# Kernel optimization log

Measured on AMD Instinct MI355X. Metric: run time of the kernel, lower is better.

The kernel has to match this reference:

```python
import jax, jax.numpy as jnp
import numpy as np
import math

QUERY_DIM = 1024
KEY_DIM = 768
VALUE_DIM = 768
NUM_HEADS = 16
HEAD_DIM = QUERY_DIM // NUM_HEADS


def setup_inputs() -> dict:
    key = jax.random.key(0)
    ks = jax.random.split(key, 11)
    B, Sq, Skv = 4, 2048, 2048
    query = jax.random.normal(ks[0], (B, Sq, QUERY_DIM), dtype=jnp.float32)
    k_in = jax.random.normal(ks[1], (B, Skv, KEY_DIM), dtype=jnp.float32)
    v_in = jax.random.normal(ks[2], (B, Skv, VALUE_DIM), dtype=jnp.float32)
    # Linear weights stored as [in, out] (y = x @ W + b), equivalent to torch's x @ W^T.
    def lin(k, fan_in, fan_out):
        bound = 1.0 / math.sqrt(fan_in)
        kw, kb = jax.random.split(k)
        W = jax.random.uniform(kw, (fan_in, fan_out), minval=-bound, maxval=bound, dtype=jnp.float32)
        b = jax.random.uniform(kb, (fan_out,), minval=-bound, maxval=bound, dtype=jnp.float32)
        return W, b
    Wq, bq = lin(ks[3], QUERY_DIM, QUERY_DIM)
    Wk, bk = lin(ks[4], KEY_DIM, QUERY_DIM)
    Wv, bv = lin(ks[5], VALUE_DIM, QUERY_DIM)
    Wo, bo = lin(ks[6], QUERY_DIM, QUERY_DIM)
    return {"query": query, "key": k_in, "value": v_in,
            "Wq": Wq, "bq": bq, "Wk": Wk, "bk": bk,
            "Wv": Wv, "bv": bv, "Wo": Wo, "bo": bo}


def reference(query, key, value, Wq, bq, Wk, bk, Wv, bv, Wo, bo):
    B, Sq, _ = query.shape
    H, D = NUM_HEADS, HEAD_DIM
    # Projections -> [B, H, S, D]
    Q = (query @ Wq + bq).reshape(B, Sq, H, D).transpose(0, 2, 1, 3)
    K = (key @ Wk + bk).reshape(B, -1, H, D).transpose(0, 2, 1, 3)
    V = (value @ Wv + bv).reshape(B, -1, H, D).transpose(0, 2, 1, 3)
    scale = 1.0 / math.sqrt(D)
    scores = jnp.einsum('bhqd,bhkd->bhqk', Q, K) * scale  # [B,H,Sq,Skv]
    weights = jax.nn.softmax(scores, axis=-1)
    attended = jnp.einsum('bhqk,bhkd->bhqd', weights, V)
    attended = attended.transpose(0, 2, 1, 3).reshape(B, Sq, H * D)
    # torch .squeeze(1): no-op since Sq > 1
    return attended @ Wo + bo
```

## Files before the change

### kernel.cpp

```cpp
#include <hip/hip_runtime.h>

#define B_ 4
#define SQ 2048
#define SKV 2048
#define DMODEL 1024
#define DKV 768
#define NH 16
#define DH 64

typedef unsigned short u16;
typedef __bf16 bf16x4 __attribute__((ext_vector_type(4)));
typedef __bf16 bf16x8 __attribute__((ext_vector_type(8)));
typedef float f32x4 __attribute__((ext_vector_type(4)));
typedef float f32x16 __attribute__((ext_vector_type(16)));

__device__ __forceinline__ u16 f2bf(float f) {
  union { __bf16 b; u16 u; } cv;
  cv.b = (__bf16)f;
  return cv.u;
}

__device__ __forceinline__ unsigned cvtpk(float lo, float hi) {
  unsigned r;
  asm("v_cvt_pk_bf16_f32 %0, %1, %2" : "=v"(r) : "v"(lo), "v"(hi));
  return r;
}

__device__ __forceinline__ float fexp2(float x) {
  float r;
  asm("v_exp_f32 %0, %1" : "=v"(r) : "v"(x));
  return r;
}

#define GLDS(gp, lp) __builtin_amdgcn_global_load_lds(                         \
    (const __attribute__((address_space(1))) unsigned*)(gp),                   \
    (__attribute__((address_space(3))) unsigned*)(lp), 16, 0, 0)


__global__ __launch_bounds__(128)
void cast3_kernel(const float* __restrict__ Aq, const float* __restrict__ Ak,
                  const float* __restrict__ Av,
                  u16* __restrict__ Qb, u16* __restrict__ Kb, u16* __restrict__ Vb) {
  const int z = blockIdx.y;
  const float* src = (z == 0) ? Aq : (z == 1) ? Ak : Av;
  u16* dst = (z == 0) ? Qb : (z == 1) ? Kb : Vb;
  const int K = (z == 0) ? DMODEL : DKV;
  const int row = blockIdx.x;
  const int c8 = threadIdx.x * 8;
  if (c8 >= K) return;
  const float* s = src + (size_t)row * K + c8;
  float4 v0 = *(const float4*)s;
  float4 v1 = *(const float4*)(s + 4);
  union { bf16x4 b[2]; uint4 u; } cv;
  cv.b[0][0] = (__bf16)v0.x; cv.b[0][1] = (__bf16)v0.y;
  cv.b[0][2] = (__bf16)v0.z; cv.b[0][3] = (__bf16)v0.w;
  cv.b[1][0] = (__bf16)v1.x; cv.b[1][1] = (__bf16)v1.y;
  cv.b[1][2] = (__bf16)v1.z; cv.b[1][3] = (__bf16)v1.w;
  int kx = c8 ^ ((row & 7) << 3);
  *(uint4*)(dst + (size_t)row * K + kx) = cv.u;
}

__global__ __launch_bounds__(256)
void wt4_kernel(const float* __restrict__ W0, const float* __restrict__ W1,
                const float* __restrict__ W2, const float* __restrict__ W3,
                u16* __restrict__ T0, u16* __restrict__ T1,
                u16* __restrict__ T2, u16* __restrict__ T3) {
  const int z = blockIdx.z;
  const float* W = (z == 0) ? W0 : (z == 1) ? W1 : (z == 2) ? W2 : W3;
  u16* T = (z == 0) ? T0 : (z == 1) ? T1 : (z == 2) ? T2 : T3;
  const int K = (z == 1 || z == 2) ? DKV : DMODEL;
  const int N = DMODEL;
  int n0 = blockIdx.x * 32, k0 = blockIdx.y * 32;
  if (k0 >= K) return;
  __shared__ float tl[32][33];
  int tx = threadIdx.x, ty = threadIdx.y;
#pragma unroll
  for (int p = 0; p < 4; ++p)
    tl[ty + 8 * p][tx] = W[(size_t)(k0 + ty + 8 * p) * N + n0 + tx];
  __syncthreads();
#pragma unroll
  for (int p = 0; p < 4; ++p) {
    int n = n0 + ty + 8 * p;
    int kx = (k0 + tx) ^ ((n & 7) << 3);
    T[(size_t)n * K + kx] = f2bf(tl[tx][ty + 8 * p]);
  }
}

__global__ __launch_bounds__(256)
void qkv_kernel(const u16* __restrict__ Qbf, const u16* __restrict__ Kbf,
                const u16* __restrict__ Vbf,
                const u16* __restrict__ Wtq, const u16* __restrict__ Wtk,
                const u16* __restrict__ Wtv,
                const float* __restrict__ bq, const float* __restrict__ bk,
                const float* __restrict__ bv,
                float sclq,
                u16* __restrict__ Qp, u16* __restrict__ Kp, u16* __restrict__ Vt) {
  __shared__ __align__(16) u16 Alds[128][64];
  __shared__ __align__(16) u16 Blds[128][64];
  const int z = blockIdx.z;
  const u16* Ab = (z == 0) ? Qbf : (z == 1) ? Kbf : Vbf;
  const u16* Wt = (z == 0) ? Wtq : (z == 1) ? Wtk : Wtv;
  const float* bias = (z == 0) ? bq : (z == 1) ? bk : bv;
  const int K = (z == 0) ? DMODEL : DKV;
  const float oscale = (z == 0) ? sclq : 1.0f;

  const int t = threadIdx.x;
  const int l = t & 63;
  const int lx = l & 15, lg = l >> 4;
  const int wid = t >> 6;
  const int wr = wid >> 1, wc = wid & 1;

  int flat = blockIdx.y * 8 + blockIdx.x;
  int by = (flat & 7) * 8 + ((flat >> 3) & 7);
  int bx = flat >> 6;
  const int m0 = by * 128, n0 = bx * 128;

  const int srow = l >> 3;
  const int scol = (l & 7) * 8;
  const int swz = (lx & 7) << 3;

  f32x4 acc[4][4];
#pragma unroll
  for (int i = 0; i < 4; ++i)
#pragma unroll
    for (int j = 0; j < 4; ++j) acc[i][j] = (f32x4){0.f, 0.f, 0.f, 0.f};

  for (int k0 = 0; k0 < K; k0 += 64) {
    __syncthreads();
#pragma unroll
    for (int j = 0; j < 4; ++j) {
      int row = wid * 32 + j * 8;
      GLDS(Wt + (size_t)(n0 + row + srow) * K + k0 + scol, &Blds[row][0]);
      GLDS(Ab + (size_t)(m0 + row + srow) * K + k0 + scol, &Alds[row][0]);
    }
    __syncthreads();
#pragma unroll
    for (int kk = 0; kk < 64; kk += 32) {
      bf16x8 af[4], bfr[4];
#pragma unroll
      for (int i = 0; i < 4; ++i)
        af[i] = *(const bf16x8*)(&Alds[wr * 64 + i * 16 + lx][(kk + lg * 8) ^ swz]);
#pragma unroll
      for (int j = 0; j < 4; ++j)
        bfr[j] = *(const bf16x8*)(&Blds[wc * 64 + j * 16 + lx][(kk + lg * 8) ^ swz]);
#pragma unroll
      for (int i = 0; i < 4; ++i)
#pragma unroll
        for (int j = 0; j < 4; ++j)
          acc[i][j] = __builtin_amdgcn_mfma_f32_16x16x32_bf16(af[i], bfr[j], acc[i][j], 0, 0, 0);
    }
  }
#pragma unroll
  for (int j = 0; j < 4; ++j) {
    int col = n0 + wc * 64 + j * 16 + lx;
    float bv = bias[col];
#pragma unroll
    for (int i = 0; i < 4; ++i) {
      int rowb = m0 + wr * 64 + i * 16 + lg * 4;
      f32x4 c = acc[i][j];
      if (z == 2) {
        int b = rowb >> 11, s = rowb & 2047;
        int h = col >> 6, d = col & 63;
        u16* vt = Vt + (size_t)((b * NH + h) * DH + d) * SKV + s;
        union { bf16x4 v; uint2 u; } cv;
        cv.v[0] = (__bf16)(c[0] + bv); cv.v[1] = (__bf16)(c[1] + bv);
        cv.v[2] = (__bf16)(c[2] + bv); cv.v[3] = (__bf16)(c[3] + bv);
        *(uint2*)vt = cv.u;
      } else {
        u16* op = (z == 0) ? Qp : Kp;
#pragma unroll
        for (int r = 0; r < 4; ++r)
          op[(size_t)(rowb + r) * DMODEL + col] = f2bf((c[r] + bv) * oscale);
      }
    }
  }
}

__global__ __launch_bounds__(256)
void oproj_kernel(const u16* __restrict__ Ab, const u16* __restrict__ Wt,
                  const float* __restrict__ bias, float* __restrict__ out_) {
  const int N = DMODEL, K = DMODEL;
  __shared__ __align__(16) u16 Alds[128][64];
  __shared__ __align__(16) u16 Blds[128][64];
  const int t = threadIdx.x;
  const int l = t & 63;
  const int lx = l & 15, lg = l >> 4;
  const int wid = t >> 6;
  const int wr = wid >> 1, wc = wid & 1;

  int flat = blockIdx.y * 8 + blockIdx.x;
  int by = (flat & 7) * 8 + ((flat >> 3) & 7);
  int bx = flat >> 6;
  const int m0 = by * 128, n0 = bx * 128;

  const int srow = l >> 3;
  const int scol = (l & 7) * 8;
  const int swz = (lx & 7) << 3;

  f32x4 acc[4][4];
#pragma unroll
  for (int i = 0; i < 4; ++i)
#pragma unroll
    for (int j = 0; j < 4; ++j) acc[i][j] = (f32x4){0.f, 0.f, 0.f, 0.f};

  for (int k0 = 0; k0 < K; k0 += 64) {
    __syncthreads();
#pragma unroll
    for (int j = 0; j < 4; ++j) {
      int row = wid * 32 + j * 8;
      GLDS(Wt + (size_t)(n0 + row + srow) * K + k0 + scol, &Blds[row][0]);
      GLDS(Ab + (size_t)(m0 + row + srow) * K + k0 + scol, &Alds[row][0]);
    }
    __syncthreads();
#pragma unroll
    for (int kk = 0; kk < 64; kk += 32) {
      bf16x8 af[4], bfr[4];
#pragma unroll
      for (int i = 0; i < 4; ++i)
        af[i] = *(const bf16x8*)(&Alds[wr * 64 + i * 16 + lx][(kk + lg * 8) ^ swz]);
#pragma unroll
      for (int j = 0; j < 4; ++j)
        bfr[j] = *(const bf16x8*)(&Blds[wc * 64 + j * 16 + lx][(kk + lg * 8) ^ swz]);
#pragma unroll
      for (int i = 0; i < 4; ++i)
#pragma unroll
        for (int j = 0; j < 4; ++j)
          acc[i][j] = __builtin_amdgcn_mfma_f32_16x16x32_bf16(af[i], bfr[j], acc[i][j], 0, 0, 0);
    }
  }
#pragma unroll
  for (int j = 0; j < 4; ++j) {
    int col = n0 + wc * 64 + j * 16 + lx;
    float bv = bias[col];
#pragma unroll
    for (int i = 0; i < 4; ++i) {
      int rowb = m0 + wr * 64 + i * 16 + lg * 4;
      f32x4 c = acc[i][j];
#pragma unroll
      for (int r = 0; r < 4; ++r)
        out_[(size_t)(rowb + r) * N + col] = c[r] + bv;
    }
  }
}

#define KVB 64
#define KP 72

__global__ __launch_bounds__(512, 2)
void attn_kernel(const u16* __restrict__ Qp, const u16* __restrict__ Kp,
                 const u16* __restrict__ Vt, u16* __restrict__ Att) {
  __shared__ __align__(16) u16 Klds[2][KVB][KP];
  __shared__ __align__(16) u16 Vlds[2][DH][KP];
  const int t = threadIdx.x;
  const int l = t & 63;
  const int ql = l & 31, hi = l >> 5;
  const int wid = t >> 6;

  const int flat = blockIdx.y * 8 + blockIdx.x;
  const int xcd = flat & 7;
  const int rest = flat >> 3;
  const int bh = xcd * 8 + (rest & 7);
  const int qb = rest >> 3;
  const int b = bh >> 4, h = bh & 15;
  const int q = qb * 256 + wid * 32 + ql;

  bf16x8 qf[4];
  const u16* qbase = Qp + (size_t)(b * SQ + q) * DMODEL + h * 64 + hi * 8;
#pragma unroll
  for (int ds = 0; ds < 4; ++ds) qf[ds] = *(const bf16x8*)(qbase + ds * 16);

  bf16x8 ones;
  {
    union { unsigned u[4]; bf16x8 v; } o;
    o.u[0] = o.u[1] = o.u[2] = o.u[3] = 0x3F803F80u;
    ones = o.v;
  }
  f32x16 z16;
#pragma unroll
  for (int r = 0; r < 16; ++r) z16[r] = 0.f;

  f32x16 acc0, acc1, sacc;
#pragma unroll
  for (int r = 0; r < 16; ++r) { acc0[r] = 0.f; acc1[r] = 0.f; sacc[r] = 0.f; }

  const int sr = t >> 3;
  const int sc = (t & 7) * 8;
  const u16* kg = Kp + (size_t)(b * SKV) * DMODEL + h * 64;
  const u16* vg = Vt + ((size_t)(b * NH + h) * DH + sr) * SKV;

  {
    uint4 k0 = *(const uint4*)(kg + (size_t)sr * DMODEL + sc);
    uint4 v0 = *(const uint4*)(vg + sc);
    *(uint4*)(&Klds[0][sr][sc]) = k0;
    *(uint4*)(&Vlds[0][sr][sc]) = v0;
  }
  int cur = 0;

  for (int kv0 = 0; kv0 < SKV; kv0 += KVB) {
    uint4 kr0, vr0;
    const bool pf = (kv0 + KVB) < SKV;
    if (pf) {
      kr0 = *(const uint4*)(kg + (size_t)(kv0 + KVB + sr) * DMODEL + sc);
      vr0 = *(const uint4*)(vg + kv0 + KVB + sc);
    }
    __syncthreads();

    f32x16 st0, st1;
    __builtin_amdgcn_s_setprio(1);
    {
      bf16x8 k0 = *(const bf16x8*)(&Klds[cur][ql][hi * 8]);
      bf16x8 k1 = *(const bf16x8*)(&Klds[cur][32 + ql][hi * 8]);
      st0 = __builtin_amdgcn_mfma_f32_32x32x16_bf16(k0, qf[0], z16, 0, 0, 0);
      st1 = __builtin_amdgcn_mfma_f32_32x32x16_bf16(k1, qf[0], z16, 0, 0, 0);
    }
#pragma unroll
    for (int ds = 1; ds < 4; ++ds) {
      bf16x8 k0 = *(const bf16x8*)(&Klds[cur][ql][ds * 16 + hi * 8]);
      bf16x8 k1 = *(const bf16x8*)(&Klds[cur][32 + ql][ds * 16 + hi * 8]);
      st0 = __builtin_amdgcn_mfma_f32_32x32x16_bf16(k0, qf[ds], st0, 0, 0, 0);
      st1 = __builtin_amdgcn_mfma_f32_32x32x16_bf16(k1, qf[ds], st1, 0, 0, 0);
    }
    __builtin_amdgcn_s_setprio(0);

#pragma unroll
    for (int r = 0; r < 16; ++r) { st0[r] = fexp2(st0[r]); st1[r] = fexp2(st1[r]); }

    __builtin_amdgcn_s_setprio(1);
#pragma unroll
    for (int tt = 0; tt < 2; ++tt) {
      const f32x16& stt = tt ? st1 : st0;
      unsigned pk[8];
#pragma unroll
      for (int j = 0; j < 8; ++j) pk[j] = cvtpk(stt[2 * j], stt[2 * j + 1]);
#pragma unroll
      for (int ksl = 0; ksl < 2; ++ksl) {
        auto wA = __builtin_amdgcn_permlane32_swap(pk[4 * ksl + 0], pk[4 * ksl + 2], false, false);
        auto wB = __builtin_amdgcn_permlane32_swap(pk[4 * ksl + 1], pk[4 * ksl + 3], false, false);
        union { unsigned w[4]; bf16x8 v; } pfr;
        pfr.w[0] = (unsigned)wA[0]; pfr.w[1] = (unsigned)wB[0];
        pfr.w[2] = (unsigned)wA[1]; pfr.w[3] = (unsigned)wB[1];
        int ks = tt * 2 + ksl;
        bf16x8 v0 = *(const bf16x8*)(&Vlds[cur][ql][ks * 16 + hi * 8]);
        bf16x8 v1 = *(const bf16x8*)(&Vlds[cur][32 + ql][ks * 16 + hi * 8]);
        acc0 = __builtin_amdgcn_mfma_f32_32x32x16_bf16(v0, pfr.v, acc0, 0, 0, 0);
        acc1 = __builtin_amdgcn_mfma_f32_32x32x16_bf16(v1, pfr.v, acc1, 0, 0, 0);
        sacc = __builtin_amdgcn_mfma_f32_32x32x16_bf16(ones, pfr.v, sacc, 0, 0, 0);
      }
    }
    __builtin_amdgcn_s_setprio(0);

    if (pf) {
      int nxt = cur ^ 1;
      *(uint4*)(&Klds[nxt][sr][sc]) = kr0;
      *(uint4*)(&Vlds[nxt][sr][sc]) = vr0;
    }
    cur ^= 1;
  }

  float inv = 1.0f / sacc[0];
  u16* ob = Att + (size_t)(b * SQ + q) * DMODEL + h * 64;
  const int oswz = (ql & 7) << 3;
#pragma unroll
  for (int dt = 0; dt < 2; ++dt) {
    const f32x16& a = dt ? acc1 : acc0;
#pragma unroll
    for (int g = 0; g < 4; ++g) {
      unsigned w0 = cvtpk(a[4 * g] * inv, a[4 * g + 1] * inv);
      unsigned w1 = cvtpk(a[4 * g + 2] * inv, a[4 * g + 3] * inv);
      *(uint2*)(ob + ((dt * 32 + g * 8 + hi * 4) ^ oswz)) = make_uint2(w0, w1);
    }
  }
}

extern "C" void kernel_launch(void* const* d_in, const int* in_sizes, int n_in,
                              void* d_out, int out_size, void* d_ws, size_t ws_size,
                              hipStream_t stream) {
  const float* query = (const float*)d_in[0];
  const float* key   = (const float*)d_in[1];
  const float* value = (const float*)d_in[2];
  const float* Wq = (const float*)d_in[3];
  const float* bq = (const float*)d_in[4];
  const float* Wk = (const float*)d_in[5];
  const float* bk = (const float*)d_in[6];
  const float* Wv = (const float*)d_in[7];
  const float* bv = (const float*)d_in[8];
  const float* Wo = (const float*)d_in[9];
  const float* bo = (const float*)d_in[10];
  float* out = (float*)d_out;

  u16* ws = (u16*)d_ws;
  const size_t MTOK = (size_t)B_ * SQ;
  u16* Qp  = ws;
  u16* Kp  = Qp + MTOK * DMODEL;
  u16* Vtb = Kp + MTOK * DMODEL;
  u16* Att = Vtb + MTOK * DMODEL;
  u16* WqT = Att + MTOK * DMODEL;
  u16* WkT = WqT + (size_t)DMODEL * DMODEL;
  u16* WvT = WkT + (size_t)DKV * DMODEL;
  u16* WoT = WvT + (size_t)DKV * DMODEL;
  u16* Qbf = Att;
  u16* Kbf = WoT + (size_t)DMODEL * DMODEL;
  u16* Vbf = Kbf + MTOK * DKV;

  const float SCL = 0.18033688011112042f;

  cast3_kernel<<<dim3(MTOK, 3), 128, 0, stream>>>(query, key, value, Qbf, Kbf, Vbf);

  dim3 tb(32, 8);
  wt4_kernel<<<dim3(DMODEL / 32, DMODEL / 32, 4), tb, 0, stream>>>(
      Wq, Wk, Wv, Wo, WqT, WkT, WvT, WoT);

  qkv_kernel<<<dim3(DMODEL / 128, MTOK / 128, 3), 256, 0, stream>>>(
      Qbf, Kbf, Vbf, WqT, WkT, WvT, bq, bk, bv, SCL, Qp, Kp, Vtb);

  attn_kernel<<<dim3(SQ / 256, B_ * NH), 512, 0, stream>>>(Qp, Kp, Vtb, Att);

  oproj_kernel<<<dim3(DMODEL / 128, MTOK / 128), 256, 0, stream>>>(Att, WoT, bo, out);
}
```

Measured before the change: 186.7 us.

## Stage K/V tiles via direct global-to-LDS loads with XOR-swizzled layout

Replaces the register-staged double-buffer prefetch of K and V tiles with direct global-to-LDS loads issued right after the barrier. The padded LDS arrays are replaced by unpadded 64x64 tiles whose 16-byte groups are XOR-swizzled by row, and the reads apply the matching swizzle. This is meant to cut VGPR pressure and the extra LDS store instructions. It relies on the async loads being complete before the next barrier.

Result: no change. 186.3 us (-0.2%).

```diff
diff --git a/kernel.cpp b/kernel.cpp
--- a/kernel.cpp
+++ b/kernel.cpp
@@ -244,13 +244,12 @@
 }
 
 #define KVB 64
-#define KP 72
 
 __global__ __launch_bounds__(512, 2)
 void attn_kernel(const u16* __restrict__ Qp, const u16* __restrict__ Kp,
                  const u16* __restrict__ Vt, u16* __restrict__ Att) {
-  __shared__ __align__(16) u16 Klds[2][KVB][KP];
-  __shared__ __align__(16) u16 Vlds[2][DH][KP];
+  __shared__ __align__(16) u16 Klds[2][64][64];
+  __shared__ __align__(16) u16 Vlds[2][64][64];
   const int t = threadIdx.x;
   const int l = t & 63;
   const int ql = l & 31, hi = l >> 5;
@@ -283,40 +282,35 @@
 #pragma unroll
   for (int r = 0; r < 16; ++r) { acc0[r] = 0.f; acc1[r] = 0.f; sacc[r] = 0.f; }
 
-  const int sr = t >> 3;
-  const int sc = (t & 7) * 8;
-  const u16* kg = Kp + (size_t)(b * SKV) * DMODEL + h * 64;
-  const u16* vg = Vt + ((size_t)(b * NH + h) * DH + sr) * SKV;
-
-  {
-    uint4 k0 = *(const uint4*)(kg + (size_t)sr * DMODEL + sc);
-    uint4 v0 = *(const uint4*)(vg + sc);
-    *(uint4*)(&Klds[0][sr][sc]) = k0;
-    *(uint4*)(&Vlds[0][sr][sc]) = v0;
-  }
+  const int srow = wid * 8 + (l >> 3);
+  const int sgr  = ((l & 7) ^ (l >> 3)) * 8;
+  const u16* kgb = Kp + (size_t)(b * SKV) * DMODEL + h * 64 + sgr;
+  const u16* vgb = Vt + ((size_t)(b * NH + h) * DH + srow) * SKV + sgr;
+  const int rsw = (ql & 7) << 3;
+
+  GLDS(kgb + (size_t)srow * DMODEL, &Klds[0][wid * 8][0]);
+  GLDS(vgb, &Vlds[0][wid * 8][0]);
   int cur = 0;
 
   for (int kv0 = 0; kv0 < SKV; kv0 += KVB) {
-    uint4 kr0, vr0;
-    const bool pf = (kv0 + KVB) < SKV;
-    if (pf) {
-      kr0 = *(const uint4*)(kg + (size_t)(kv0 + KVB + sr) * DMODEL + sc);
-      vr0 = *(const uint4*)(vg + kv0 + KVB + sc);
-    }
     __syncthreads();
+    if (kv0 + KVB < SKV) {
+      GLDS(kgb + (size_t)(kv0 + KVB + srow) * DMODEL, &Klds[cur ^ 1][wid * 8][0]);
+      GLDS(vgb + kv0 + KVB, &Vlds[cur ^ 1][wid * 8][0]);
+    }
 
     f32x16 st0, st1;
     __builtin_amdgcn_s_setprio(1);
     {
-      bf16x8 k0 = *(const bf16x8*)(&Klds[cur][ql][hi * 8]);
-      bf16x8 k1 = *(const bf16x8*)(&Klds[cur][32 + ql][hi * 8]);
+      bf16x8 k0 = *(const bf16x8*)(&Klds[cur][ql][(hi * 8) ^ rsw]);
+      bf16x8 k1 = *(const bf16x8*)(&Klds[cur][32 + ql][(hi * 8) ^ rsw]);
       st0 = __builtin_amdgcn_mfma_f32_32x32x16_bf16(k0, qf[0], z16, 0, 0, 0);
       st1 = __builtin_amdgcn_mfma_f32_32x32x16_bf16(k1, qf[0], z16, 0, 0, 0);
     }
 #pragma unroll
     for (int ds = 1; ds < 4; ++ds) {
-      bf16x8 k0 = *(const bf16x8*)(&Klds[cur][ql][ds * 16 + hi * 8]);
-      bf16x8 k1 = *(const bf16x8*)(&Klds[cur][32 + ql][ds * 16 + hi * 8]);
+      bf16x8 k0 = *(const bf16x8*)(&Klds[cur][ql][(ds * 16 + hi * 8) ^ rsw]);
+      bf16x8 k1 = *(const bf16x8*)(&Klds[cur][32 + ql][(ds * 16 + hi * 8) ^ rsw]);
       st0 = __builtin_amdgcn_mfma_f32_32x32x16_bf16(k0, qf[ds], st0, 0, 0, 0);
       st1 = __builtin_amdgcn_mfma_f32_32x32x16_bf16(k1, qf[ds], st1, 0, 0, 0);
     }
@@ -340,8 +334,8 @@
         pfr.w[0] = (unsigned)wA[0]; pfr.w[1] = (unsigned)wB[0];
         pfr.w[2] = (unsigned)wA[1]; pfr.w[3] = (unsigned)wB[1];
         int ks = tt * 2 + ksl;
-        bf16x8 v0 = *(const bf16x8*)(&Vlds[cur][ql][ks * 16 + hi * 8]);
-        bf16x8 v1 = *(const bf16x8*)(&Vlds[cur][32 + ql][ks * 16 + hi * 8]);
+        bf16x8 v0 = *(const bf16x8*)(&Vlds[cur][ql][(ks * 16 + hi * 8) ^ rsw]);
+        bf16x8 v1 = *(const bf16x8*)(&Vlds[cur][32 + ql][(ks * 16 + hi * 8) ^ rsw]);
         acc0 = __builtin_amdgcn_mfma_f32_32x32x16_bf16(v0, pfr.v, acc0, 0, 0, 0);
         acc1 = __builtin_amdgcn_mfma_f32_32x32x16_bf16(v1, pfr.v, acc1, 0, 0, 0);
         sacc = __builtin_amdgcn_mfma_f32_32x32x16_bf16(ones, pfr.v, sacc, 0, 0, 0);
@@ -349,11 +343,6 @@
     }
     __builtin_amdgcn_s_setprio(0);
 
-    if (pf) {
-      int nxt = cur ^ 1;
-      *(uint4*)(&Klds[nxt][sr][sc]) = kr0;
-      *(uint4*)(&Vlds[nxt][sr][sc]) = vr0;
-    }
     cur ^= 1;
   }
 
```
